# Performance work log

Hardware: AMD Instinct MI355X
Metric: run time of the kernel (lower is better)

The kernel has to match this reference:

```python
import jax, jax.numpy as jnp
import numpy as np

D_MODEL = 1024
N_HEADS = 16
HEAD_DIM = D_MODEL // N_HEADS
SEQ_LEN = 2048
D_FF = 4 * D_MODEL
LCC_SCALE = 0.1
LN_EPS = 1e-5
NORM_EPS = 1e-12  # F.normalize eps


def _layer_norm(x, g, b):
    mu = jnp.mean(x, axis=-1, keepdims=True)
    var = jnp.mean(jnp.square(x - mu), axis=-1, keepdims=True)
    return (x - mu) * jax.lax.rsqrt(var + LN_EPS) * g + b


def setup_inputs() -> dict:
    key = jax.random.key(0)
    ks = jax.random.split(key, 8)
    s = 0.02  # weight init scale
    return {
        "x": jax.random.normal(ks[0], (SEQ_LEN, D_MODEL), jnp.float32),
        "lcc_values": jax.random.uniform(ks[1], (SEQ_LEN,), jnp.float32),
        "w_qkv": jax.random.normal(ks[2], (D_MODEL, 3 * D_MODEL), jnp.float32) * s,
        "b_qkv": jnp.zeros((3 * D_MODEL,), jnp.float32),
        "w_out": jax.random.normal(ks[3], (D_MODEL, D_MODEL), jnp.float32) * s,
        "b_out": jnp.zeros((D_MODEL,), jnp.float32),
        "ln1_g": jnp.ones((D_MODEL,), jnp.float32),
        "ln1_b": jnp.zeros((D_MODEL,), jnp.float32),
        "ln2_g": jnp.ones((D_MODEL,), jnp.float32),
        "ln2_b": jnp.zeros((D_MODEL,), jnp.float32),
        "w_ff1": jax.random.normal(ks[4], (D_MODEL, D_FF), jnp.float32) * s,
        "b_ff1": jnp.zeros((D_FF,), jnp.float32),
        "w_ff2": jax.random.normal(ks[5], (D_FF, D_MODEL), jnp.float32) * s,
        "b_ff2": jnp.zeros((D_MODEL,), jnp.float32),
    }


def reference(x, lcc_values, w_qkv, b_qkv, w_out, b_out, ln1_g, ln1_b,
              ln2_g, ln2_b, w_ff1, b_ff1, w_ff2, b_ff2):
    L = x.shape[0]
    scaling = HEAD_DIM ** -0.5

    normed = _layer_norm(x, ln1_g, ln1_b)
    qkv = normed @ w_qkv + b_qkv                      # [L, 3D]
    qkv = qkv.reshape(L, 3, N_HEADS, HEAD_DIM)
    q = jnp.transpose(qkv[:, 0], (1, 0, 2))           # [H, L, d]
    k = jnp.transpose(qkv[:, 1], (1, 0, 2))
    v = jnp.transpose(qkv[:, 2], (1, 0, 2))

    # cosine attention: L2-normalize q, k
    q = q / jnp.maximum(jnp.linalg.norm(q, axis=-1, keepdims=True), NORM_EPS)
    k = k / jnp.maximum(jnp.linalg.norm(k, axis=-1, keepdims=True), NORM_EPS)
    q = q * scaling

    scores = jnp.einsum('hld,hmd->hlm', q, k)         # [H, L, L]
    bias = (lcc_values[:, None] + lcc_values[None, :]) * 0.5 * LCC_SCALE
    scores = jnp.clip(scores + bias[None], -10.0, 10.0)
    probs = jax.nn.softmax(scores, axis=-1)

    attn = jnp.einsum('hlm,hmd->hld', probs, v)       # [H, L, d]
    attn = jnp.transpose(attn, (1, 0, 2)).reshape(L, D_MODEL)
    x = x + (attn @ w_out + b_out)

    normed2 = _layer_norm(x, ln2_g, ln2_b)
    h = jax.nn.gelu(normed2 @ w_ff1 + b_ff1, approximate=False)
    x = x + (h @ w_ff2 + b_ff2)
    return x
```

## Files before the change

kernel.cpp:

```cpp
#include <hip/hip_runtime.h>
#include <hip/hip_bf16.h>

#define D_MODEL 1024
#define SEQ 2048
#define NH 16
#define HD 64
#define DFF 4096

typedef __attribute__((ext_vector_type(8))) __bf16 bf16x8;
typedef __attribute__((ext_vector_type(4))) float f32x4;

__device__ __forceinline__ unsigned short f2bf(float f) {
    union { float f; unsigned u; } v; v.f = f;
    unsigned r = v.u + 0x7fffu + ((v.u >> 16) & 1u);
    return (unsigned short)(r >> 16);
}
__device__ __forceinline__ unsigned pack2(float a, float b) {
    return (unsigned)f2bf(a) | ((unsigned)f2bf(b) << 16);
}
__device__ __forceinline__ float bf2f(unsigned short u) {
    union { unsigned u; float f; } v; v.u = ((unsigned)u) << 16;
    return v.f;
}
__device__ __forceinline__ bf16x8 ld_frag(const unsigned short* p) {
    union { uint4 u; bf16x8 b; } c;
    c.u = *(const uint4*)p;
    return c.b;
}

typedef __attribute__((address_space(3))) unsigned lds_u32;
typedef const __attribute__((address_space(1))) unsigned glob_u32;
__device__ __forceinline__ void gl_lds16(const unsigned short* g, unsigned short* l) {
    __builtin_amdgcn_global_load_lds((glob_u32*)g, (lds_u32*)l, 16, 0, 0);
}

#define MFMA16(a,b,c) __builtin_amdgcn_mfma_f32_16x16x32_bf16(a,b,c,0,0,0)

__global__ __launch_bounds__(256) void wcast_all(const float* __restrict__ wq, const float* __restrict__ wo,
                                                 const float* __restrict__ wf1, const float* __restrict__ wf2,
                                                 unsigned short* __restrict__ oq, unsigned short* __restrict__ oo,
                                                 unsigned short* __restrict__ of1, unsigned short* __restrict__ of2) {
    __shared__ unsigned short lt[64][72];
    int id = blockIdx.x;
    const float* W; unsigned short* O; int K, N, nb, kb;
    if (id < 768)       { W = wq;  O = oq;  K = 1024; N = 3072; nb = id % 48; kb = id / 48; }
    else if (id < 1024) { id -= 768;  W = wo;  O = oo;  K = 1024; N = 1024; nb = id & 15; kb = id >> 4; }
    else if (id < 2048) { id -= 1024; W = wf1; O = of1; K = 1024; N = 4096; nb = id & 63; kb = id >> 6; }
    else                { id -= 2048; W = wf2; O = of2; K = 4096; N = 1024; nb = id & 15; kb = id >> 4; }
    int t = threadIdx.x;
    int r = t >> 2, c0 = (t & 3) << 4;
    const float* src = W + (size_t)(kb*64 + r) * N + nb*64 + c0;
    float4 f0 = ((const float4*)src)[0];
    float4 f1 = ((const float4*)src)[1];
    float4 f2 = ((const float4*)src)[2];
    float4 f3 = ((const float4*)src)[3];
    unsigned* dst = (unsigned*)&lt[r][c0];
    dst[0]=pack2(f0.x,f0.y); dst[1]=pack2(f0.z,f0.w);
    dst[2]=pack2(f1.x,f1.y); dst[3]=pack2(f1.z,f1.w);
    dst[4]=pack2(f2.x,f2.y); dst[5]=pack2(f2.z,f2.w);
    dst[6]=pack2(f3.x,f3.y); dst[7]=pack2(f3.z,f3.w);
    __syncthreads();
    int n_ = t >> 2, k0 = (t & 3) << 4;
    unsigned obuf[8];
#pragma unroll
    for (int i = 0; i < 8; i++)
        obuf[i] = (unsigned)lt[k0 + 2*i][n_] | ((unsigned)lt[k0 + 2*i + 1][n_] << 16);
    unsigned short* out = O + (size_t)(nb*64 + n_) * K + kb*64 + k0;
    ((uint4*)out)[0] = *(uint4*)&obuf[0];
    ((uint4*)out)[1] = *(uint4*)&obuf[4];
}

__global__ __launch_bounds__(256) void ln_kernel(const float* __restrict__ x,
                                                 const float* __restrict__ g,
                                                 const float* __restrict__ b,
                                                 unsigned short* __restrict__ out) {
    int row = blockIdx.x, t = threadIdx.x;
    float4 v = ((const float4*)(x + (size_t)row * D_MODEL))[t];
    float s  = v.x + v.y + v.z + v.w;
    float sq = v.x*v.x + v.y*v.y + v.z*v.z + v.w*v.w;
#pragma unroll
    for (int m = 1; m < 64; m <<= 1) { s += __shfl_xor(s, m, 64); sq += __shfl_xor(sq, m, 64); }
    __shared__ float ls[4], lq[4];
    int wave = t >> 6, lane = t & 63;
    if (lane == 0) { ls[wave] = s; lq[wave] = sq; }
    __syncthreads();
    s  = ls[0]+ls[1]+ls[2]+ls[3];
    sq = lq[0]+lq[1]+lq[2]+lq[3];
    float mu  = s * (1.0f / D_MODEL);
    float var = sq * (1.0f / D_MODEL) - mu * mu;
    float rs  = rsqrtf(var + 1e-5f);
    int c = t * 4;
    float y0 = (v.x - mu) * rs * g[c+0] + b[c+0];
    float y1 = (v.y - mu) * rs * g[c+1] + b[c+1];
    float y2 = (v.z - mu) * rs * g[c+2] + b[c+2];
    float y3 = (v.w - mu) * rs * g[c+3] + b[c+3];
    unsigned* o = (unsigned*)(out + (size_t)row * D_MODEL + c);
    o[0] = pack2(y0, y1); o[1] = pack2(y2, y3);
}

__global__ __launch_bounds__(256) void reduce_ln(const float* __restrict__ x,
                                                 const float* __restrict__ bout,
                                                 const unsigned short* __restrict__ parts,
                                                 const float* __restrict__ g,
                                                 const float* __restrict__ b,
                                                 float* __restrict__ x1,
                                                 unsigned short* __restrict__ x2n) {
    int row = blockIdx.x, t = threadIdx.x;
    int i = row * 256 + t;
    float4 v = ((const float4*)x)[i];
    float4 bb = ((const float4*)bout)[t];
    v.x += bb.x; v.y += bb.y; v.z += bb.z; v.w += bb.w;
#pragma unroll
    for (int p = 0; p < 4; p++) {
        ushort4 u = ((const ushort4*)(parts + (size_t)p * SEQ * D_MODEL))[i];
        v.x += bf2f(u.x); v.y += bf2f(u.y); v.z += bf2f(u.z); v.w += bf2f(u.w);
    }
    ((float4*)x1)[i] = v;
    float s  = v.x + v.y + v.z + v.w;
    float sq = v.x*v.x + v.y*v.y + v.z*v.z + v.w*v.w;
#pragma unroll
    for (int m = 1; m < 64; m <<= 1) { s += __shfl_xor(s, m, 64); sq += __shfl_xor(sq, m, 64); }
    __shared__ float ls[4], lq[4];
    int wave = t >> 6, lane = t & 63;
    if (lane == 0) { ls[wave] = s; lq[wave] = sq; }
    __syncthreads();
    s  = ls[0]+ls[1]+ls[2]+ls[3];
    sq = lq[0]+lq[1]+lq[2]+lq[3];
    float mu  = s * (1.0f / D_MODEL);
    float var = sq * (1.0f / D_MODEL) - mu * mu;
    float rs  = rsqrtf(var + 1e-5f);
    int c = t * 4;
    float y0 = (v.x - mu) * rs * g[c+0] + b[c+0];
    float y1 = (v.y - mu) * rs * g[c+1] + b[c+1];
    float y2 = (v.z - mu) * rs * g[c+2] + b[c+2];
    float y3 = (v.w - mu) * rs * g[c+3] + b[c+3];
    unsigned* o = (unsigned*)(x2n + (size_t)row * D_MODEL + c);
    o[0] = pack2(y0, y1); o[1] = pack2(y2, y3);
}

__global__ __launch_bounds__(256) void reduce_ff2(const float* __restrict__ res,
                                                  const float* __restrict__ bias,
                                                  const unsigned short* __restrict__ parts,
                                                  float* __restrict__ out) {
    int i = blockIdx.x * 256 + threadIdx.x;
    float4 r = ((const float4*)res)[i];
    float4 b = ((const float4*)bias)[i & (D_MODEL/4 - 1)];
    r.x += b.x; r.y += b.y; r.z += b.z; r.w += b.w;
#pragma unroll
    for (int p = 0; p < 4; p++) {
        ushort4 u = ((const ushort4*)(parts + (size_t)p * SEQ * D_MODEL))[i];
        r.x += bf2f(u.x); r.y += bf2f(u.y); r.z += bf2f(u.z); r.w += bf2f(u.w);
    }
    ((float4*)out)[i] = r;
}

#define BMh 256
#define BNh 256
#define SMEM8_U16 65536

__device__ __forceinline__ void acc_init8(f32x4 acc[8][4]) {
    f32x4 z = {0.f, 0.f, 0.f, 0.f};
#pragma unroll
    for (int i = 0; i < 8; i++)
#pragma unroll
        for (int j = 0; j < 4; j++) acc[i][j] = z;
}

__device__ __forceinline__ void issue_half(const unsigned short* gA0, const unsigned short* gA1,
                                           const unsigned short* gB0, const unsigned short* gB1,
                                           unsigned short* smem, int s,
                                           int dA0, int dA1, int dB0, int dB1) {
    unsigned short* db = smem + ((s >> 1) & 1) * 32768 + (s & 1) * 8192;
    gl_lds16(gA0 + s*32, db + dA0);
    gl_lds16(gA1 + s*32, db + dA1);
    gl_lds16(gB0 + s*32, db + 16384 + dB0);
    gl_lds16(gB1 + s*32, db + 16384 + dB1);
}

__device__ __forceinline__ void gemm_core8ph(const unsigned short* __restrict__ A,
                                             const unsigned short* __restrict__ Bt,
                                             int K, int K0, int KS, int bm, int bn,
                                             unsigned short* smem, f32x4 acc[8][4],
                                             int w, int lane) {
    int quad = lane >> 4, lr = lane & 15;
    int wm = w >> 2, wn = w & 3;
    int t = w*64 + lane;
    int srow = t >> 2, sch = t & 3;
    int r0 = srow, r1 = 128 + srow;
    int sc = sch ^ (r0 & 3);
    const unsigned short* gA0 = A  + (size_t)(bm*BMh + r0) * K + K0 + sc*8;
    const unsigned short* gA1 = A  + (size_t)(bm*BMh + r1) * K + K0 + sc*8;
    const unsigned short* gB0 = Bt + (size_t)(bn*BNh + r0) * K + K0 + sc*8;
    const unsigned short* gB1 = Bt + (size_t)(bn*BNh + r1) * K + K0 + sc*8;
    int dA0 = r0*32 + sch*8, dA1 = r1*32 + sch*8;
    int foA[8], foB[4];
#pragma unroll
    for (int i = 0; i < 8; i++) { int ra = wm*128 + i*16 + lr; foA[i] = ra*32 + ((quad ^ (ra & 3)))*8; }
#pragma unroll
    for (int j = 0; j < 4; j++) { int rb = wn*64 + j*16 + lr; foB[j] = rb*32 + ((quad ^ (rb & 3)))*8; }

    int T2 = KS >> 5;
    issue_half(gA0, gA1, gB0, gB1, smem, 0, dA0, dA1, dA0, dA1);
    issue_half(gA0, gA1, gB0, gB1, smem, 1, dA0, dA1, dA0, dA1);
    for (int s = 0; s < T2; s++) {
        if (s + 1 < T2) asm volatile("s_waitcnt vmcnt(4)" ::: "memory");
        else            asm volatile("s_waitcnt vmcnt(0)" ::: "memory");
        __builtin_amdgcn_s_barrier();
        if (s + 2 < T2) issue_half(gA0, gA1, gB0, gB1, smem, s + 2, dA0, dA1, dA0, dA1);
        const unsigned short* sa = smem + ((s >> 1) & 1) * 32768 + (s & 1) * 8192;
        const unsigned short* sb = sa + 16384;
        bf16x8 bfr[4], af0[4], af1[4];
#pragma unroll
        for (int j = 0; j < 4; j++) bfr[j] = ld_frag(sb + foB[j]);
#pragma unroll
        for (int i = 0; i < 4; i++) af0[i] = ld_frag(sa + foA[i]);
        __builtin_amdgcn_s_setprio(1);
#pragma unroll
        for (int i = 0; i < 4; i++)
#pragma unroll
            for (int j = 0; j < 4; j++)
                acc[i][j] = MFMA16(af0[i], bfr[j], acc[i][j]);
        __builtin_amdgcn_s_setprio(0);
#pragma unroll
        for (int i = 0; i < 4; i++) af1[i] = ld_frag(sa + foA[4 + i]);
        __builtin_amdgcn_s_setprio(1);
#pragma unroll
        for (int i = 0; i < 4; i++)
#pragma unroll
            for (int j = 0; j < 4; j++)
                acc[4 + i][j] = MFMA16(af1[i], bfr[j], acc[4 + i][j]);
        __builtin_amdgcn_s_setprio(0);
    }
}

__global__ __launch_bounds__(512, 2) void k_gemm_ff1(const unsigned short* __restrict__ A,
                                                     const unsigned short* __restrict__ Bt,
                                                     const float* __restrict__ bias,
                                                     unsigned short* __restrict__ C,
                                                     int M, int N, int K) {
    __shared__ unsigned short smem[SMEM8_U16];
    int t = threadIdx.x, w = t >> 6, lane = t & 63;
    int bn = blockIdx.x, bm = blockIdx.y;
    int quad = lane >> 4, lr = lane & 15;
    f32x4 acc[8][4];
    acc_init8(acc);
    gemm_core8ph(A, Bt, K, 0, K, bm, bn, smem, acc, w, lane);
    int wm = w >> 2, wn = w & 3;
#pragma unroll
    for (int j = 0; j < 4; j++) {
        int col = bn*BNh + wn*64 + j*16 + lr;
        float bvv = bias[col];
#pragma unroll
        for (int i = 0; i < 8; i++) {
            int row0 = bm*BMh + wm*128 + i*16 + quad*4;
#pragma unroll
            for (int r = 0; r < 4; r++) {
                float v = acc[i][j][r] + bvv;
                v = 0.5f * v * (1.0f + erff(v * 0.70710678118654752f));
                C[(size_t)(row0 + r) * N + col] = f2bf(v);
            }
        }
    }
}

__global__ __launch_bounds__(512, 2) void k_gemm_ff2(const unsigned short* __restrict__ A,
                                                     const unsigned short* __restrict__ Bt,
                                                     unsigned short* __restrict__ C,
                                                     int M, int N, int K) {
    __shared__ unsigned short smem[SMEM8_U16];
    int t = threadIdx.x, w = t >> 6, lane = t & 63;
    int bn = blockIdx.x, bm = blockIdx.y, kz = blockIdx.z;
    int quad = lane >> 4, lr = lane & 15;
    int KS = K >> 2;
    f32x4 acc[8][4];
    acc_init8(acc);
    gemm_core8ph(A, Bt, K, kz*KS, KS, bm, bn, smem, acc, w, lane);
    int wm = w >> 2, wn = w & 3;
    unsigned short* P = C + (size_t)kz * M * N;
#pragma unroll
    for (int j = 0; j < 4; j++) {
        int col = bn*BNh + wn*64 + j*16 + lr;
#pragma unroll
        for (int i = 0; i < 8; i++) {
            int row0 = bm*BMh + wm*128 + i*16 + quad*4;
#pragma unroll
            for (int r = 0; r < 4; r++)
                P[(size_t)(row0 + r) * N + col] = f2bf(acc[i][j][r]);
        }
    }
}

#define TMg 128
#define TNg 128
#define HALFg ((TMg + TNg) * 64)
#define SMEM_U16 (2 * HALFg)
__device__ __forceinline__ void gemm_core512(const unsigned short* __restrict__ A,
                                             const unsigned short* __restrict__ Bt,
                                             int K, int K0, int KS, int bm, int bn,
                                             unsigned short* smem, f32x4 acc[4][4],
                                             int w, int lane) {
    int quad = lane >> 4, lr = lane & 15;
    int kg = w >> 2;
    const unsigned short* pa[2]; const unsigned short* pb[2];
    int aoff[2], boff[2];
#pragma unroll
    for (int i = 0; i < 2; i++) {
        int rl = i*64 + w*8 + (lane >> 3);
        int sc = (lane & 7) ^ (rl & 7);
        pa[i] = A  + (size_t)(bm*TMg + rl) * K + K0 + sc*8;
        pb[i] = Bt + (size_t)(bn*TNg + rl) * K + K0 + sc*8;
        aoff[i] = (i*64 + w*8) * 64;
        boff[i] = TMg*64 + (i*64 + w*8) * 64;
    }
    int wr = ((w >> 1) & 1) * 64, wc = (w & 1) * 64;
    int foA[4], foB[4];
#pragma unroll
    for (int i = 0; i < 4; i++) {
        int ra = wr + i*16 + lr;
        foA[i] = ra*64 + (((quad + 4*kg) ^ (ra & 7)))*8;
        int rb = wc + i*16 + lr;
        foB[i] = TMg*64 + rb*64 + (((quad + 4*kg) ^ (rb & 7)))*8;
    }
#pragma unroll
    for (int i = 0; i < 2; i++) { gl_lds16(pa[i], smem + aoff[i]); gl_lds16(pb[i], smem + boff[i]); }
    int bo = 0;
    int T = KS >> 6;
    for (int t = 0; t < T; t++) {
        __syncthreads();
        if (t + 1 < T) {
            int nb = bo ^ HALFg;
#pragma unroll
            for (int i = 0; i < 2; i++) {
                gl_lds16(pa[i] + (t+1)*64, smem + nb + aoff[i]);
                gl_lds16(pb[i] + (t+1)*64, smem + nb + boff[i]);
            }
        }
        const unsigned short* s = smem + bo;
        bf16x8 af[4], bfr[4];
#pragma unroll
        for (int i = 0; i < 4; i++) af[i] = ld_frag(s + foA[i]);
#pragma unroll
        for (int j = 0; j < 4; j++) bfr[j] = ld_frag(s + foB[j]);
        __builtin_amdgcn_s_setprio(1);
#pragma unroll
        for (int i = 0; i < 4; i++)
#pragma unroll
            for (int j = 0; j < 4; j++)
                acc[i][j] = MFMA16(af[i], bfr[j], acc[i][j]);
        __builtin_amdgcn_s_setprio(0);
        bo ^= HALFg;
    }
}

__device__ __forceinline__ void acc_init(f32x4 acc[4][4]) {
    f32x4 z = {0.f, 0.f, 0.f, 0.f};
#pragma unroll
    for (int i = 0; i < 4; i++)
#pragma unroll
        for (int j = 0; j < 4; j++) acc[i][j] = z;
}

__device__ __forceinline__ void acc_merge_split(unsigned short* smem, f32x4 acc[4][4],
                                                int w, int lane) {
    float* X = (float*)smem;
    int kg = w >> 2, p = w & 3, quad = lane >> 4, lr = lane & 15;
    if (kg) {
#pragma unroll
        for (int i = 0; i < 4; i++) {
            f32x4 t0 = acc[i][0]; acc[i][0] = acc[i][2]; acc[i][2] = t0;
            f32x4 t1 = acc[i][1]; acc[i][1] = acc[i][3]; acc[i][3] = t1;
        }
    }
    __syncthreads();
    int g = (kg ^ 1) * 2;
#pragma unroll
    for (int i = 0; i < 4; i++)
#pragma unroll
        for (int r = 0; r < 4; r++) {
            int ro = (i*16 + r*4 + quad)*16 + lr;
            X[(p*4 + g    )*1024 + ro] = acc[i][2][r];
            X[(p*4 + g + 1)*1024 + ro] = acc[i][3][r];
        }
    __syncthreads();
    int k = kg * 2;
#pragma unroll
    for (int i = 0; i < 4; i++)
#pragma unroll
        for (int r = 0; r < 4; r++) {
            int ro = (i*16 + r*4 + quad)*16 + lr;
            acc[i][0][r] += X[(p*4 + k    )*1024 + ro];
            acc[i][1][r] += X[(p*4 + k + 1)*1024 + ro];
        }
}

__global__ __launch_bounds__(512, 4) void k_gemm_qkv(const unsigned short* __restrict__ A,
                                                     const unsigned short* __restrict__ Bt,
                                                     const float* __restrict__ bias,
                                                     unsigned short* __restrict__ qn,
                                                     unsigned short* __restrict__ kn,
                                                     unsigned short* __restrict__ vt) {
    __shared__ unsigned short smem[SMEM_U16];
    int t = threadIdx.x;
    int bn = blockIdx.x, bm = blockIdx.y;
    int w = t >> 6, lane = t & 63;
    int quad = lane >> 4, lr = lane & 15;
    f32x4 acc[4][4];
    acc_init(acc);
    gemm_core512(A, Bt, 1024, 0, 1024, bm, bn, smem, acc, w, lane);

    float* X = (float*)smem;
    int kg = w >> 2, p = w & 3;
    __syncthreads();
    if (kg == 1) {
#pragma unroll
        for (int j = 0; j < 4; j++) {
            float* slot = X + (p*4 + j)*1024;
#pragma unroll
            for (int i = 0; i < 4; i++)
#pragma unroll
                for (int r = 0; r < 4; r++)
                    slot[(i*16 + r*4 + quad)*16 + lr] = acc[i][j][r];
        }
    }
    __syncthreads();
    int wr = ((w >> 1) & 1) * 64, wc = (w & 1) * 64;
    int sec = bn >> 3, hp = bn & 7;
    if (kg == 0) {
#pragma unroll
        for (int j = 0; j < 4; j++) {
            const float* slot = X + (p*4 + j)*1024;
            float bv = bias[bn*TNg + wc + j*16 + lr];
#pragma unroll
            for (int i = 0; i < 4; i++)
#pragma unroll
                for (int r = 0; r < 4; r++)
                    acc[i][j][r] += slot[(i*16 + r*4 + quad)*16 + lr] + bv;
        }
    }

    if (sec < 2) {
        if (kg == 0) {
            int h = hp*2 + (w & 1);
            unsigned short* dst = (sec == 0) ? qn : kn;
            float mul = (sec == 0) ? 0.125f : 1.0f;
#pragma unroll
            for (int i = 0; i < 4; i++)
#pragma unroll
                for (int r = 0; r < 4; r++) {
                    float ss = 0.f;
#pragma unroll
                    for (int j = 0; j < 4; j++) ss += acc[i][j][r]*acc[i][j][r];
                    ss += __shfl_xor(ss, 1, 64); ss += __shfl_xor(ss, 2, 64);
                    ss += __shfl_xor(ss, 4, 64); ss += __shfl_xor(ss, 8, 64);
                    float scale = mul / fmaxf(sqrtf(ss), 1e-12f);
                    int row = bm*TMg + wr + i*16 + quad*4 + r;
                    size_t base = ((size_t)h*SEQ + row) * HD;
#pragma unroll
                    for (int j = 0; j < 4; j++)
                        dst[base + j*16 + lr] = f2bf(acc[i][j][r] * scale);
                }
        }
    } else {
        __syncthreads();
        unsigned short (*lv)[136] = (unsigned short (*)[136])smem;
        if (kg == 0) {
#pragma unroll
            for (int i = 0; i < 4; i++)
#pragma unroll
                for (int j = 0; j < 4; j++)
#pragma unroll
                    for (int r = 0; r < 4; r++)
                        lv[wc + j*16 + lr][wr + i*16 + quad*4 + r] = f2bf(acc[i][j][r]);
        }
        __syncthreads();
        int d = t >> 2, l0 = (t & 3) * 32;
        unsigned short* ov = vt + ((size_t)(hp*128 + d)) * SEQ + bm*TMg + l0;
#pragma unroll
        for (int c = 0; c < 4; c++)
            ((uint4*)ov)[c] = *(uint4*)&lv[d][l0 + c*8];
    }
}

template<int SPLITK>
__device__ __forceinline__ void gemm_part512(const unsigned short* A, const unsigned short* Bt,
                                             unsigned short* C, int M, int N, int K) {
    __shared__ unsigned short smem[SMEM_U16];
    int t = threadIdx.x;
    int bn = blockIdx.x, bm = blockIdx.y, kz = blockIdx.z;
    int w = t >> 6, lane = t & 63;
    int quad = lane >> 4, lr = lane & 15;
    int KS = K / SPLITK;
    f32x4 acc[4][4];
    acc_init(acc);
    gemm_core512(A, Bt, K, kz*KS, KS, bm, bn, smem, acc, w, lane);
    acc_merge_split(smem, acc, w, lane);
    int kg = w >> 2, wr = ((w >> 1) & 1) * 64, wc = (w & 1) * 64;
    unsigned short* P = C + (size_t)kz * M * N;
    int col0 = bn*TNg + wc + (kg*2)*16 + lr;
    int col1 = col0 + 16;
#pragma unroll
    for (int i = 0; i < 4; i++) {
        int row0 = bm*TMg + wr + i*16 + quad*4;
#pragma unroll
        for (int r = 0; r < 4; r++) {
            P[(size_t)(row0 + r) * N + col0] = f2bf(acc[i][0][r]);
            P[(size_t)(row0 + r) * N + col1] = f2bf(acc[i][1][r]);
        }
    }
}
__global__ __launch_bounds__(512, 4) void k_gemm_op(const unsigned short* A, const unsigned short* Bt,
                                                    unsigned short* C, int M, int N, int K) {
    gemm_part512<4>(A, Bt, C, M, N, K);
}

#define KSPLIT 2
#define KTILES (SEQ / 64 / KSPLIT)
__global__ __launch_bounds__(256) void attn_kernel(const unsigned short* __restrict__ qn,
                                                   const unsigned short* __restrict__ kn,
                                                   const unsigned short* __restrict__ vt,
                                                   const float* __restrict__ lcc,
                                                   float* __restrict__ num_ws,
                                                   float* __restrict__ den_ws) {
    __shared__ unsigned short lQP[64*64];
    __shared__ unsigned short lK[2][64*64];
    __shared__ unsigned short lV[2][64*64];
    int h = blockIdx.x, qb = blockIdx.y, kz = blockIdx.z;
    int t = threadIdx.x;
    int wave = t >> 6, lane = t & 63, quad = lane >> 4, lr = lane & 15;
    int r0 = lane >> 3;
    int ch = lane & 7;

    const unsigned short* kn0 = kn + (size_t)h*SEQ*HD + (size_t)kz*(SEQ/KSPLIT)*HD;
    const unsigned short* vt0 = vt + (size_t)h*HD*SEQ + kz*(SEQ/KSPLIT);
    const float* lcc0 = lcc + kz*(SEQ/KSPLIT);

#pragma unroll
    for (int i = 0; i < 2; i++) {
        int rl = wave*16 + i*8 + r0;
        int ss = ch ^ (rl & 7);
        gl_lds16(qn + ((size_t)h*SEQ + qb*64 + rl)*HD + ss*8, lQP + (wave*16 + i*8)*64);
        gl_lds16(kn0 + (size_t)rl*HD + ss*8,                  lK[0] + (wave*16 + i*8)*64);
        gl_lds16(vt0 + (size_t)rl*SEQ + ss*8,                 lV[0] + (wave*16 + i*8)*64);
    }
    __syncthreads();

    bf16x8 aq0 = ld_frag(lQP + (wave*16 + lr)*64 + ((quad     ^ (lr & 7)))*8);
    bf16x8 aq1 = ld_frag(lQP + (wave*16 + lr)*64 + (((quad+4) ^ (lr & 7)))*8);

    f32x4 z = {0.f, 0.f, 0.f, 0.f};
    f32x4 oacc[4]; oacc[0]=z; oacc[1]=z; oacc[2]=z; oacc[3]=z;
    float den[4] = {0.f, 0.f, 0.f, 0.f};

    int cur = 0;
    for (int kb = 0; kb < KTILES; kb++) {
        if (kb + 1 < KTILES) {
            int nxt = cur ^ 1;
#pragma unroll
            for (int i = 0; i < 2; i++) {
                int rl = wave*16 + i*8 + r0;
                int ss = ch ^ (rl & 7);
                gl_lds16(kn0 + (size_t)(kb+1)*64*HD + (size_t)rl*HD + ss*8,
                         lK[nxt] + (wave*16 + i*8)*64);
                gl_lds16(vt0 + (size_t)rl*SEQ + (kb+1)*64 + ss*8,
                         lV[nxt] + (wave*16 + i*8)*64);
            }
        }
        float lmv[4];
#pragma unroll
        for (int j = 0; j < 4; j++) lmv[j] = 0.05f * lcc0[kb*64 + j*16 + lr];

        __builtin_amdgcn_s_setprio(1);
        const unsigned short* Kc = lK[cur];
#pragma unroll
        for (int j = 0; j < 4; j++) {
            bf16x8 b0 = ld_frag(Kc + (j*16 + lr)*64 + ((quad     ^ (lr & 7)))*8);
            bf16x8 b1 = ld_frag(Kc + (j*16 + lr)*64 + (((quad+4) ^ (lr & 7)))*8);
            f32x4 s = z;
            s = MFMA16(aq0, b0, s);
            s = MFMA16(aq1, b1, s);
#pragma unroll
            for (int r = 0; r < 4; r++) {
                float p = __expf(s[r] + lmv[j]);
                den[r] += p;
                int prow = wave*16 + quad*4 + r;
                lQP[prow*64 + (((2*j + (lr >> 3)) ^ (prow & 7)))*8 + (lr & 7)] = f2bf(p);
            }
        }
        bf16x8 ap0 = ld_frag(lQP + (wave*16 + lr)*64 + ((quad     ^ (lr & 7)))*8);
        bf16x8 ap1 = ld_frag(lQP + (wave*16 + lr)*64 + (((quad+4) ^ (lr & 7)))*8);
        const unsigned short* Vc = lV[cur];
#pragma unroll
        for (int j2 = 0; j2 < 4; j2++) {
            bf16x8 b0 = ld_frag(Vc + (j2*16 + lr)*64 + ((quad     ^ (lr & 7)))*8);
            bf16x8 b1 = ld_frag(Vc + (j2*16 + lr)*64 + (((quad+4) ^ (lr & 7)))*8);
            oacc[j2] = MFMA16(ap0, b0, oacc[j2]);
            oacc[j2] = MFMA16(ap1, b1, oacc[j2]);
        }
        __builtin_amdgcn_s_setprio(0);
        __syncthreads();
        cur ^= 1;
    }
#pragma unroll
    for (int r = 0; r < 4; r++)
#pragma unroll
        for (int m = 1; m < 16; m <<= 1) den[r] += __shfl_xor(den[r], m, 64);

    float* nump = num_ws + (((size_t)(h*32 + qb)) * KSPLIT + kz) * 4096;
#pragma unroll
    for (int j2 = 0; j2 < 4; j2++)
#pragma unroll
        for (int r = 0; r < 4; r++)
            nump[(wave*16 + quad*4 + r) * 64 + j2*16 + lr] = oacc[j2][r];
    if (lr == 0) {
        float* denp = den_ws + (((size_t)(h*32 + qb)) * KSPLIT + kz) * 64;
#pragma unroll
        for (int r = 0; r < 4; r++) denp[wave*16 + quad*4 + r] = den[r];
    }
}

__global__ __launch_bounds__(256) void attn_comb(const float* __restrict__ num_ws,
                                                 const float* __restrict__ den_ws,
                                                 unsigned short* __restrict__ attn) {
    int hq = blockIdx.x;
    int h = hq >> 5, qb = hq & 31;
    int t = threadIdx.x;
    int row = t >> 2, col0 = (t & 3) << 4;
    const float* n0 = num_ws + ((size_t)hq * KSPLIT) * 4096 + row*64 + col0;
    const float* n1 = n0 + 4096;
    float d = den_ws[(size_t)hq * KSPLIT * 64 + row] + den_ws[((size_t)hq * KSPLIT + 1) * 64 + row];
    float inv = 1.0f / d;
    unsigned ob[8];
#pragma unroll
    for (int i = 0; i < 4; i++) {
        float4 a = ((const float4*)n0)[i];
        float4 b = ((const float4*)n1)[i];
        ob[2*i]   = pack2((a.x + b.x) * inv, (a.y + b.y) * inv);
        ob[2*i+1] = pack2((a.z + b.z) * inv, (a.w + b.w) * inv);
    }
    unsigned short* op = attn + (size_t)(qb*64 + row) * D_MODEL + h*64 + col0;
    ((uint4*)op)[0] = *(uint4*)&ob[0];
    ((uint4*)op)[1] = *(uint4*)&ob[4];
}

extern "C" void kernel_launch(void* const* d_in, const int* in_sizes, int n_in,
                              void* d_out, int out_size, void* d_ws, size_t ws_size,
                              hipStream_t stream) {
    const float* x      = (const float*)d_in[0];
    const float* lcc    = (const float*)d_in[1];
    const float* w_qkv  = (const float*)d_in[2];
    const float* b_qkv  = (const float*)d_in[3];
    const float* w_out  = (const float*)d_in[4];
    const float* b_out  = (const float*)d_in[5];
    const float* ln1_g  = (const float*)d_in[6];
    const float* ln1_b  = (const float*)d_in[7];
    const float* ln2_g  = (const float*)d_in[8];
    const float* ln2_b  = (const float*)d_in[9];
    const float* w_ff1  = (const float*)d_in[10];
    const float* b_ff1  = (const float*)d_in[11];
    const float* w_ff2  = (const float*)d_in[12];
    const float* b_ff2  = (const float*)d_in[13];

    char* ws = (char*)d_ws;
    unsigned short* wtq  = (unsigned short*)(ws);
    unsigned short* wto  = (unsigned short*)(ws + 6291456);
    unsigned short* wtf1 = (unsigned short*)(ws + 8388608);
    unsigned short* wtf2 = (unsigned short*)(ws + 16777216);
    unsigned short* xn   = (unsigned short*)(ws + 25165824);
    float*          x1   = (float*)(ws + 29360128);
    float*          numw = (float*)(ws + 29360128);
    float*          denw = (float*)(ws + 46137344);
    unsigned short* hbuf = (unsigned short*)(ws + 37748736);
    unsigned short* pOP  = (unsigned short*)(ws + 37748736);
    unsigned short* qnb  = (unsigned short*)(ws + 54525952);
    unsigned short* knb  = (unsigned short*)(ws + 58720256);
    unsigned short* vtb  = (unsigned short*)(ws + 62914560);
    unsigned short* pFF2 = (unsigned short*)(ws);
    unsigned short* attnb = xn;
    unsigned short* x2n  = qnb;
    float* outp = (float*)d_out;


    wcast_all<<<3072, 256, 0, stream>>>(w_qkv, w_out, w_ff1, w_ff2, wtq, wto, wtf1, wtf2);
    ln_kernel<<<SEQ, 256, 0, stream>>>(x, ln1_g, ln1_b, xn);
    k_gemm_qkv<<<dim3(24, 16), 512, 0, stream>>>(xn, wtq, b_qkv, qnb, knb, vtb);
    attn_kernel<<<dim3(16, 32, KSPLIT), 256, 0, stream>>>(qnb, knb, vtb, lcc, numw, denw);
    attn_comb<<<512, 256, 0, stream>>>(numw, denw, attnb);
    k_gemm_op<<<dim3(8, 16, 4), 512, 0, stream>>>(attnb, wto, pOP, SEQ, 1024, 1024);
    reduce_ln<<<SEQ, 256, 0, stream>>>(x, b_out, pOP, ln2_g, ln2_b, x1, x2n);
    k_gemm_ff1<<<dim3(16, 8), 512, 0, stream>>>(x2n, wtf1, b_ff1, hbuf, SEQ, 4096, 1024);
    k_gemm_ff2<<<dim3(4, 8, 4), 512, 0, stream>>>(hbuf, wtf2, pFF2, SEQ, 1024, 4096);
    reduce_ff2<<<SEQ*D_MODEL/1024, 256, 0, stream>>>(x1, b_ff2, pFF2, outp);
}
```

Measured before the change: 286.3 us.

## Shrink FF GEMM tiles to 128x256 with BK=64 double-buffered pipeline

Replaces the 256x256 tile, BK=32 four-stage FF GEMM core with a 128x256 tile using BK=64 double buffering, an 8-way XOR swizzle and a barrier before refilling the consumed buffer. This halves per-thread accumulators and doubles the grid for FF1 (256 blocks) and FF2 (256 blocks), improving occupancy and CU fill on the many-CU device. In exchange it lowers arithmetic intensity per tile and adds an extra barrier per K step.

Measured after the change: 257.0 us. 1.11x faster.

```diff
diff --git a/kernel.cpp b/kernel.cpp
--- a/kernel.cpp
+++ b/kernel.cpp
@@ -154,83 +154,89 @@
     ((float4*)out)[i] = r;
 }
 
-#define BMh 256
-#define BNh 256
-#define SMEM8_U16 65536
-
-__device__ __forceinline__ void acc_init8(f32x4 acc[8][4]) {
-    f32x4 z = {0.f, 0.f, 0.f, 0.f};
-#pragma unroll
-    for (int i = 0; i < 8; i++)
-#pragma unroll
-        for (int j = 0; j < 4; j++) acc[i][j] = z;
-}
-
-__device__ __forceinline__ void issue_half(const unsigned short* gA0, const unsigned short* gA1,
-                                           const unsigned short* gB0, const unsigned short* gB1,
-                                           unsigned short* smem, int s,
-                                           int dA0, int dA1, int dB0, int dB1) {
-    unsigned short* db = smem + ((s >> 1) & 1) * 32768 + (s & 1) * 8192;
-    gl_lds16(gA0 + s*32, db + dA0);
-    gl_lds16(gA1 + s*32, db + dA1);
-    gl_lds16(gB0 + s*32, db + 16384 + dB0);
-    gl_lds16(gB1 + s*32, db + 16384 + dB1);
-}
-
-__device__ __forceinline__ void gemm_core8ph(const unsigned short* __restrict__ A,
+#define BMf 128
+#define BNf 256
+#define FBUF_U16 ((BMf + BNf) * 64)
+#define FSMEM_U16 (2 * FBUF_U16)
+__device__ __forceinline__ void gemm_core_ff(const unsigned short* __restrict__ A,
                                              const unsigned short* __restrict__ Bt,
                                              int K, int K0, int KS, int bm, int bn,
-                                             unsigned short* smem, f32x4 acc[8][4],
+                                             unsigned short* smem, f32x4 acc[4][4],
                                              int w, int lane) {
     int quad = lane >> 4, lr = lane & 15;
     int wm = w >> 2, wn = w & 3;
-    int t = w*64 + lane;
-    int srow = t >> 2, sch = t & 3;
-    int r0 = srow, r1 = 128 + srow;
-    int sc = sch ^ (r0 & 3);
-    const unsigned short* gA0 = A  + (size_t)(bm*BMh + r0) * K + K0 + sc*8;
-    const unsigned short* gA1 = A  + (size_t)(bm*BMh + r1) * K + K0 + sc*8;
-    const unsigned short* gB0 = Bt + (size_t)(bn*BNh + r0) * K + K0 + sc*8;
-    const unsigned short* gB1 = Bt + (size_t)(bn*BNh + r1) * K + K0 + sc*8;
-    int dA0 = r0*32 + sch*8, dA1 = r1*32 + sch*8;
-    int foA[8], foB[4];
-#pragma unroll
-    for (int i = 0; i < 8; i++) { int ra = wm*128 + i*16 + lr; foA[i] = ra*32 + ((quad ^ (ra & 3)))*8; }
-#pragma unroll
-    for (int j = 0; j < 4; j++) { int rb = wn*64 + j*16 + lr; foB[j] = rb*32 + ((quad ^ (rb & 3)))*8; }
-
-    int T2 = KS >> 5;
-    issue_half(gA0, gA1, gB0, gB1, smem, 0, dA0, dA1, dA0, dA1);
-    issue_half(gA0, gA1, gB0, gB1, smem, 1, dA0, dA1, dA0, dA1);
-    for (int s = 0; s < T2; s++) {
-        if (s + 1 < T2) asm volatile("s_waitcnt vmcnt(4)" ::: "memory");
-        else            asm volatile("s_waitcnt vmcnt(0)" ::: "memory");
+    const unsigned short* pa[2]; int da[2];
+#pragma unroll
+    for (int i = 0; i < 2; i++) {
+        int rl = w*16 + i*8 + (lane >> 3);
+        int sc = (lane & 7) ^ (rl & 7);
+        pa[i] = A + (size_t)(bm*BMf + rl) * K + K0 + sc*8;
+        da[i] = (w*16 + i*8) * 64;
+    }
+    const unsigned short* pb[4]; int db[4];
+#pragma unroll
+    for (int i = 0; i < 4; i++) {
+        int rl = w*32 + i*8 + (lane >> 3);
+        int sc = (lane & 7) ^ (rl & 7);
+        pb[i] = Bt + (size_t)(bn*BNf + rl) * K + K0 + sc*8;
+        db[i] = BMf*64 + (w*32 + i*8) * 64;
+    }
+    int foA[2][4], foB[2][4];
+#pragma unroll
+    for (int i = 0; i < 4; i++) {
+        int ra = wm*64 + i*16 + lr;
+        foA[0][i] = ra*64 + ((quad     ^ (ra & 7)))*8;
+        foA[1][i] = ra*64 + (((quad+4) ^ (ra & 7)))*8;
+        int rb = wn*64 + i*16 + lr;
+        foB[0][i] = BMf*64 + rb*64 + ((quad     ^ (rb & 7)))*8;
+        foB[1][i] = BMf*64 + rb*64 + (((quad+4) ^ (rb & 7)))*8;
+    }
+    int T = KS >> 6;
+#pragma unroll
+    for (int t = 0; t < 2; t++) {
+        unsigned short* s = smem + t * FBUF_U16;
+#pragma unroll
+        for (int i = 0; i < 2; i++) gl_lds16(pa[i] + t*64, s + da[i]);
+#pragma unroll
+        for (int i = 0; i < 4; i++) gl_lds16(pb[i] + t*64, s + db[i]);
+    }
+    for (int t = 0; t < T; t++) {
+        if (t + 1 < T) asm volatile("s_waitcnt vmcnt(6)" ::: "memory");
+        else           asm volatile("s_waitcnt vmcnt(0)" ::: "memory");
         __builtin_amdgcn_s_barrier();
-        if (s + 2 < T2) issue_half(gA0, gA1, gB0, gB1, smem, s + 2, dA0, dA1, dA0, dA1);
-        const unsigned short* sa = smem + ((s >> 1) & 1) * 32768 + (s & 1) * 8192;
-        const unsigned short* sb = sa + 16384;
-        bf16x8 bfr[4], af0[4], af1[4];
-#pragma unroll
-        for (int j = 0; j < 4; j++) bfr[j] = ld_frag(sb + foB[j]);
-#pragma unroll
-        for (int i = 0; i < 4; i++) af0[i] = ld_frag(sa + foA[i]);
-        __builtin_amdgcn_s_setprio(1);
-#pragma unroll
-        for (int i = 0; i < 4; i++)
-#pragma unroll
-            for (int j = 0; j < 4; j++)
-                acc[i][j] = MFMA16(af0[i], bfr[j], acc[i][j]);
-        __builtin_amdgcn_s_setprio(0);
-#pragma unroll
-        for (int i = 0; i < 4; i++) af1[i] = ld_frag(sa + foA[4 + i]);
-        __builtin_amdgcn_s_setprio(1);
-#pragma unroll
-        for (int i = 0; i < 4; i++)
-#pragma unroll
-            for (int j = 0; j < 4; j++)
-                acc[4 + i][j] = MFMA16(af1[i], bfr[j], acc[4 + i][j]);
-        __builtin_amdgcn_s_setprio(0);
-    }
+        const unsigned short* s = smem + (t & 1) * FBUF_U16;
+#pragma unroll
+        for (int h = 0; h < 2; h++) {
+            bf16x8 af[4], bfr[4];
+#pragma unroll
+            for (int i = 0; i < 4; i++) af[i]  = ld_frag(s + foA[h][i]);
+#pragma unroll
+            for (int j = 0; j < 4; j++) bfr[j] = ld_frag(s + foB[h][j]);
+            __builtin_amdgcn_s_setprio(1);
+#pragma unroll
+            for (int i = 0; i < 4; i++)
+#pragma unroll
+                for (int j = 0; j < 4; j++)
+                    acc[i][j] = MFMA16(af[i], bfr[j], acc[i][j]);
+            __builtin_amdgcn_s_setprio(0);
+        }
+        __builtin_amdgcn_s_barrier();
+        if (t + 2 < T) {
+            unsigned short* sn = smem + (t & 1) * FBUF_U16;
+#pragma unroll
+            for (int i = 0; i < 2; i++) gl_lds16(pa[i] + (t+2)*64, sn + da[i]);
+#pragma unroll
+            for (int i = 0; i < 4; i++) gl_lds16(pb[i] + (t+2)*64, sn + db[i]);
+        }
+    }
+}
+
+__device__ __forceinline__ void acc_init(f32x4 acc[4][4]) {
+    f32x4 z = {0.f, 0.f, 0.f, 0.f};
+#pragma unroll
+    for (int i = 0; i < 4; i++)
+#pragma unroll
+        for (int j = 0; j < 4; j++) acc[i][j] = z;
 }
 
 __global__ __launch_bounds__(512, 2) void k_gemm_ff1(const unsigned short* __restrict__ A,
@@ -238,21 +244,21 @@
                                                      const float* __restrict__ bias,
                                                      unsigned short* __restrict__ C,
                                                      int M, int N, int K) {
-    __shared__ unsigned short smem[SMEM8_U16];
+    __shared__ unsigned short smem[FSMEM_U16];
     int t = threadIdx.x, w = t >> 6, lane = t & 63;
     int bn = blockIdx.x, bm = blockIdx.y;
     int quad = lane >> 4, lr = lane & 15;
-    f32x4 acc[8][4];
-    acc_init8(acc);
-    gemm_core8ph(A, Bt, K, 0, K, bm, bn, smem, acc, w, lane);
+    f32x4 acc[4][4];
+    acc_init(acc);
+    gemm_core_ff(A, Bt, K, 0, K, bm, bn, smem, acc, w, lane);
     int wm = w >> 2, wn = w & 3;
 #pragma unroll
     for (int j = 0; j < 4; j++) {
-        int col = bn*BNh + wn*64 + j*16 + lr;
+        int col = bn*BNf + wn*64 + j*16 + lr;
         float bvv = bias[col];
 #pragma unroll
-        for (int i = 0; i < 8; i++) {
-            int row0 = bm*BMh + wm*128 + i*16 + quad*4;
+        for (int i = 0; i < 4; i++) {
+            int row0 = bm*BMf + wm*64 + i*16 + quad*4;
 #pragma unroll
             for (int r = 0; r < 4; r++) {
                 float v = acc[i][j][r] + bvv;
@@ -267,22 +273,22 @@
                                                      const unsigned short* __restrict__ Bt,
                                                      unsigned short* __restrict__ C,
                                                      int M, int N, int K) {
-    __shared__ unsigned short smem[SMEM8_U16];
+    __shared__ unsigned short smem[FSMEM_U16];
     int t = threadIdx.x, w = t >> 6, lane = t & 63;
     int bn = blockIdx.x, bm = blockIdx.y, kz = blockIdx.z;
     int quad = lane >> 4, lr = lane & 15;
     int KS = K >> 2;
-    f32x4 acc[8][4];
-    acc_init8(acc);
-    gemm_core8ph(A, Bt, K, kz*KS, KS, bm, bn, smem, acc, w, lane);
+    f32x4 acc[4][4];
+    acc_init(acc);
+    gemm_core_ff(A, Bt, K, kz*KS, KS, bm, bn, smem, acc, w, lane);
     int wm = w >> 2, wn = w & 3;
     unsigned short* P = C + (size_t)kz * M * N;
 #pragma unroll
     for (int j = 0; j < 4; j++) {
-        int col = bn*BNh + wn*64 + j*16 + lr;
-#pragma unroll
-        for (int i = 0; i < 8; i++) {
-            int row0 = bm*BMh + wm*128 + i*16 + quad*4;
+        int col = bn*BNf + wn*64 + j*16 + lr;
+#pragma unroll
+        for (int i = 0; i < 4; i++) {
+            int row0 = bm*BMf + wm*64 + i*16 + quad*4;
 #pragma unroll
             for (int r = 0; r < 4; r++)
                 P[(size_t)(row0 + r) * N + col] = f2bf(acc[i][j][r]);
@@ -350,14 +356,6 @@
         __builtin_amdgcn_s_setprio(0);
         bo ^= HALFg;
     }
-}
-
-__device__ __forceinline__ void acc_init(f32x4 acc[4][4]) {
-    f32x4 z = {0.f, 0.f, 0.f, 0.f};
-#pragma unroll
-    for (int i = 0; i < 4; i++)
-#pragma unroll
-        for (int j = 0; j < 4; j++) acc[i][j] = z;
 }
 
 __device__ __forceinline__ void acc_merge_split(unsigned short* smem, f32x4 acc[4][4],
@@ -687,7 +685,7 @@
     attn_comb<<<512, 256, 0, stream>>>(numw, denw, attnb);
     k_gemm_op<<<dim3(8, 16, 4), 512, 0, stream>>>(attnb, wto, pOP, SEQ, 1024, 1024);
     reduce_ln<<<SEQ, 256, 0, stream>>>(x, b_out, pOP, ln2_g, ln2_b, x1, x2n);
-    k_gemm_ff1<<<dim3(16, 8), 512, 0, stream>>>(x2n, wtf1, b_ff1, hbuf, SEQ, 4096, 1024);
-    k_gemm_ff2<<<dim3(4, 8, 4), 512, 0, stream>>>(hbuf, wtf2, pFF2, SEQ, 1024, 4096);
+    k_gemm_ff1<<<dim3(16, 16), 512, 0, stream>>>(x2n, wtf1, b_ff1, hbuf, SEQ, 4096, 1024);
+    k_gemm_ff2<<<dim3(4, 16, 4), 512, 0, stream>>>(hbuf, wtf2, pFF2, SEQ, 1024, 4096);
     reduce_ff2<<<SEQ*D_MODEL/1024, 256, 0, stream>>>(x1, b_ff2, pFF2, outp);
 }
```
